# Optimization experiments

Hardware: AMD Instinct MI355X
Metric: run time of the kernel (lower is better)

Reference implementation:

```python
import jax, jax.numpy as jnp
import numpy as np
from jax import lax

B, C, H, W = 4, 512, 64, 64
C8 = C // 8
OUT = 256
BN_EPS = 1e-5


def setup_inputs() -> dict:
    key = jax.random.key(0)
    ks = jax.random.split(key, 12)
    s = lambda k, shape, fan: jax.random.normal(k, shape, jnp.float32) * (1.0 / np.sqrt(fan))
    return {
        "x": jax.random.normal(ks[0], (B, C, H, W), jnp.float32),
        "wq": s(ks[1], (C8, C), C), "bq": jnp.zeros((C8,), jnp.float32),
        "wk": s(ks[2], (C8, C), C), "bk": jnp.zeros((C8,), jnp.float32),
        "wv": s(ks[3], (C, C), C),  "bv": jnp.zeros((C,), jnp.float32),
        "ca_w1": s(ks[4], (C8, C), C),
        "ca_w2": s(ks[5], (C, C8), C8),
        "conv_w": s(ks[6], (OUT, C, 3, 3), C * 9),
        "bn_gamma": jnp.ones((OUT,), jnp.float32),
        "bn_beta": jnp.zeros((OUT,), jnp.float32),
        "bn_mean": jnp.zeros((OUT,), jnp.float32),
        "bn_var": jnp.ones((OUT,), jnp.float32),
    }


def reference(x, wq, bq, wk, bk, wv, bv, ca_w1, ca_w2, conv_w,
              bn_gamma, bn_beta, bn_mean, bn_var):
    b, c, h, w = x.shape
    n = h * w
    xf = x.reshape(b, c, n)  # [B,C,N]

    # ---- Position attention ----
    q = jnp.einsum('qc,bcn->bnq', wq, xf) + bq            # [B,N,C8]
    k = jnp.einsum('kc,bcn->bkn', wk, xf) + bk[:, None]   # [B,C8,N]
    energy = jnp.einsum('bnq,bqm->bnm', q, k)             # [B,N,N]
    attn = jax.nn.softmax(energy, axis=-1)
    v = jnp.einsum('vc,bcn->bvn', wv, xf) + bv[:, None]   # [B,C,N]
    # torch: bmm(value, attention^T) -> out[b,c,m] = sum_n v[b,c,n]*attn[b,m,n]
    pa = jnp.einsum('bcn,bmn->bcm', v, attn).reshape(b, c, h, w) + x

    # ---- Channel attention (SE-style, avg+max pooled, shared MLP) ----
    avg = jnp.mean(pa, axis=(2, 3))   # [B,C]
    mx = jnp.max(pa, axis=(2, 3))     # [B,C]
    fc = lambda z: jnp.einsum('oc,bc->bo', ca_w2,
                              jax.nn.relu(jnp.einsum('hc,bc->bh', ca_w1, z)))
    scale = jax.nn.sigmoid(fc(avg) + fc(mx))[:, :, None, None]
    ca = scale * pa

    # ---- Conv 3x3 + BN (eval mode) + ReLU ----
    y = lax.conv_general_dilated(ca, conv_w, (1, 1), 'SAME',
                                 dimension_numbers=('NCHW', 'OIHW', 'NCHW'))
    inv = lax.rsqrt(bn_var + BN_EPS)
    y = (y - bn_mean[:, None, None]) * (inv * bn_gamma)[:, None, None] + bn_beta[:, None, None]
    return jax.nn.relu(y)
```

## Files before the change

### kernel.cpp

```cpp
#include <hip/hip_runtime.h>

#define NB 4
#define CIN 512
#define NPIX 4096
#define CQK 64
#define COUT 256
#define PPIX 4356

typedef __bf16 bh16;
typedef _Float16 fh16;
typedef __attribute__((ext_vector_type(8))) __bf16 bf16x8;
typedef __attribute__((ext_vector_type(8))) _Float16 f16x8;
typedef __attribute__((ext_vector_type(16))) float f32x16;

#define AS1 __attribute__((address_space(1)))
#define AS3 __attribute__((address_space(3)))

__device__ __forceinline__ void glds16(const void* g, void* l) {
  __builtin_amdgcn_global_load_lds((const AS1 unsigned int*)g, (AS3 unsigned int*)l, 16, 0, 0);
}

__global__ __launch_bounds__(256) void transpose_bf_k(const float* __restrict__ src,
                                                      bh16* __restrict__ dst,
                                                      int rows, int cols) {
  __shared__ float tile[32][33];
  const int b = blockIdx.z;
  const int c0 = blockIdx.x * 32;
  const int r0 = blockIdx.y * 32;
  const float* s = src + (size_t)b * rows * cols;
  bh16* d = dst + (size_t)b * rows * cols;
  const int tx = threadIdx.x, ty = threadIdx.y;
#pragma unroll
  for (int i = 0; i < 32; i += 8)
    tile[ty + i][tx] = s[(size_t)(r0 + ty + i) * cols + (c0 + tx)];
  __syncthreads();
#pragma unroll
  for (int i = 0; i < 32; i += 8)
    d[(size_t)(c0 + ty + i) * rows + (r0 + tx)] = (bh16)tile[tx][ty + i];
}

__global__ __launch_bounds__(256) void wcast_k(const float* __restrict__ wq,
                                               const float* __restrict__ wk,
                                               const float* __restrict__ wv,
                                               const float* __restrict__ bq,
                                               const float* __restrict__ bk,
                                               bh16* __restrict__ Wqk,
                                               bh16* __restrict__ wvb,
                                               float* __restrict__ bias128) {
  const int idx = blockIdx.x * 256 + threadIdx.x;
  if (idx < 65536) {
    Wqk[idx] = (bh16)(idx < 32768 ? wq[idx] : wk[idx - 32768]);
  } else {
    const int j = idx - 65536;
    wvb[j] = (bh16)wv[j];
  }
  if (idx < 128) bias128[idx] = idx < 64 ? bq[idx] : bk[idx - 64];
}

__global__ __launch_bounds__(256) void qk_proj_k(const bh16* __restrict__ xTb,
                                                 const bh16* __restrict__ Wqk,
                                                 const float* __restrict__ bias128,
                                                 bh16* __restrict__ Qb,
                                                 bh16* __restrict__ Kf) {
  const int blk = blockIdx.x;
  const int t = threadIdx.x;
  const int w = t >> 6, l31 = t & 31, hi = (t & 63) >> 5;
  __shared__ __align__(16) bh16 As[2][64 * 64];
  f32x16 acc[2];
#pragma unroll
  for (int nt = 0; nt < 2; nt++)
#pragma unroll
    for (int r = 0; r < 16; r++) acc[nt][r] = 0.0f;

#define QK_STAGE(kc, buf)                                                           \
  {                                                                                 \
    _Pragma("unroll") for (int i = 0; i < 2; i++) {                                 \
      const int s = i * 256 + t;                                                    \
      const int n = s >> 3, slot = s & 7;                                           \
      glds16(xTb + (size_t)(blk * 64 + n) * CIN + (kc) * 64 + (((slot + n) & 7) * 8), \
             &As[buf][(size_t)(i * 256 + w * 64) * 8]);                             \
    }                                                                               \
  }

  QK_STAGE(0, 0);
  __syncthreads();
  for (int kc = 0; kc < 8; kc++) {
    if (kc < 7) QK_STAGE(kc + 1, (kc + 1) & 1);
    const bh16* as = As[kc & 1];
#pragma unroll
    for (int ks = 0; ks < 4; ks++) {
      const bf16x8 bfr = *(const bf16x8*)(Wqk + (size_t)(w * 32 + l31) * CIN + kc * 64 + ks * 16 + hi * 8);
      const int kk = ks * 2 + hi;
#pragma unroll
      for (int nt = 0; nt < 2; nt++) {
        const int n = nt * 32 + l31;
        const bf16x8 a = *(const bf16x8*)&as[(size_t)(n * 8 + ((kk - n) & 7)) * 8];
        acc[nt] = __builtin_amdgcn_mfma_f32_32x32x16_bf16(a, bfr, acc[nt], 0, 0, 0);
      }
    }
    __syncthreads();
  }
#undef QK_STAGE
  const int o = w * 32 + l31;
  const float bo = bias128[o];
  if (w < 2) {
#pragma unroll
    for (int nt = 0; nt < 2; nt++)
#pragma unroll
      for (int r = 0; r < 16; r++) {
        const int nloc = nt * 32 + (r & 3) + 8 * (r >> 2) + 4 * hi;
        Qb[(size_t)(blk * 64 + nloc) * 64 + o] = (bh16)(acc[nt][r] + bo);
      }
  } else {
    const int b = blk >> 6, jtile = blk & 63;
    const int k = o - 64, kg = k >> 3, k7 = k & 7;
    bh16* kdst = Kf + (((size_t)(b * 64 + jtile) * 8 + kg) * 64) * 8 + k7;
#pragma unroll
    for (int nt = 0; nt < 2; nt++)
#pragma unroll
      for (int r = 0; r < 16; r++) {
        const int j = nt * 32 + (r & 3) + 8 * (r >> 2) + 4 * hi;
        kdst[(size_t)j * 8] = (bh16)(acc[nt][r] + bo);
      }
  }
}

__global__ __launch_bounds__(256) void v_proj_k(const bh16* __restrict__ xTb,
                                                const bh16* __restrict__ wvb,
                                                const float* __restrict__ bv,
                                                bh16* __restrict__ Vf) {
  const int nblk = blockIdx.x;
  const int cblk = blockIdx.y;
  const int b = blockIdx.z;
  const int t = threadIdx.x;
  const int w = t >> 6, l31 = t & 31, hi = (t & 63) >> 5;
  __shared__ __align__(16) bh16 Bs[2][256 * 64];
  f32x16 acc[2][2];
#pragma unroll
  for (int mt = 0; mt < 2; mt++)
#pragma unroll
    for (int nt = 0; nt < 2; nt++)
#pragma unroll
      for (int r = 0; r < 16; r++) acc[mt][nt][r] = 0.0f;

#define V_STAGE(kc, buf)                                                              \
  {                                                                                   \
    _Pragma("unroll") for (int i = 0; i < 8; i++) {                                   \
      const int s = i * 256 + t;                                                      \
      const int n = s >> 3, slot = s & 7;                                             \
      glds16(xTb + (size_t)(b * NPIX + nblk * 256 + n) * CIN + (kc) * 64 + (((slot + n) & 7) * 8), \
             &Bs[buf][(size_t)(i * 256 + w * 64) * 8]);                               \
    }                                                                                 \
  }

  V_STAGE(0, 0);
  __syncthreads();
  for (int kc = 0; kc < 8; kc++) {
    if (kc < 7) V_STAGE(kc + 1, (kc + 1) & 1);
    const bh16* bs = Bs[kc & 1];
#pragma unroll
    for (int ks = 0; ks < 4; ks++) {
      const int kk = ks * 2 + hi;
      bf16x8 a[2], bfr[2];
#pragma unroll
      for (int mt = 0; mt < 2; mt++)
        a[mt] = *(const bf16x8*)(wvb + (size_t)(cblk * 64 + mt * 32 + l31) * CIN + kc * 64 + ks * 16 + hi * 8);
#pragma unroll
      for (int nt = 0; nt < 2; nt++) {
        const int n = w * 64 + nt * 32 + l31;
        bfr[nt] = *(const bf16x8*)&bs[(size_t)(n * 8 + ((kk - n) & 7)) * 8];
      }
#pragma unroll
      for (int mt = 0; mt < 2; mt++)
#pragma unroll
        for (int nt = 0; nt < 2; nt++)
          acc[mt][nt] = __builtin_amdgcn_mfma_f32_32x32x16_bf16(a[mt], bfr[nt], acc[mt][nt], 0, 0, 0);
    }
    __syncthreads();
  }
#undef V_STAGE
  const int ntile0 = nblk * 4 + w;
#pragma unroll
  for (int mt = 0; mt < 2; mt++)
#pragma unroll
    for (int r = 0; r < 16; r++) {
      const int c = cblk * 64 + mt * 32 + (r & 3) + 8 * (r >> 2) + 4 * hi;
      const float bvc = bv[c];
#pragma unroll
      for (int nt = 0; nt < 2; nt++) {
        const int nl = nt * 32 + l31;
        Vf[(((size_t)(b * 64 + ntile0) * 8 + (nl >> 3)) * 512 + c) * 8 + (nl & 7)] =
            (bh16)(acc[mt][nt][r] + bvc);
      }
    }
}

__global__ __launch_bounds__(256, 2) void attn1p_k(const bh16* __restrict__ Qb,
                                                   const bh16* __restrict__ Kf,
                                                   const bh16* __restrict__ Vf,
                                                   const float* __restrict__ x,
                                                   float* __restrict__ pa) {
  const int id = blockIdx.x + 2 * (blockIdx.y + 64 * blockIdx.z);
  const int b = (id & 7) >> 1;
  const int cblk = id & 1;
  const int mblk = (id >> 3) * 64;
  const int t = threadIdx.x;
  const int w = t >> 6, l31 = t & 31, hi = (t >> 5) & 1;
  const int jhalf = w & 1, mhalf = w >> 1;
  __shared__ __align__(16) bh16 Ps[2][8 * 64 * 8];
  __shared__ float lred[4][32];
  __shared__ float linvL[64];

  bf16x8 qf[4];
  {
    const bh16* qrow = Qb + (size_t)(b * NPIX + mblk + mhalf * 32 + l31) * 64;
#pragma unroll
    for (int ks = 0; ks < 4; ks++) qf[ks] = *(const bf16x8*)(qrow + ks * 16 + hi * 8);
  }
  const bh16* kfb = Kf + (size_t)b * (64 * 8 * 64 * 8);
  const bh16* vfb = Vf + (size_t)b * (64 * 8 * 512 * 8);
  const int cbase = cblk * 256 + w * 64;

  f32x16 acc[2][2];
#pragma unroll
  for (int mt = 0; mt < 2; mt++)
#pragma unroll
    for (int ct = 0; ct < 2; ct++)
#pragma unroll
      for (int r = 0; r < 16; r++) acc[mt][ct][r] = 0.0f;
  float lsum = 0.0f;

  bf16x8 kf[4], vf[4][2];
#pragma unroll
  for (int ks = 0; ks < 4; ks++) {
    kf[ks] = *(const bf16x8*)(kfb + (((size_t)0 * 8 + ks * 2 + hi) * 64 + jhalf * 32 + l31) * 8);
#pragma unroll
    for (int ct = 0; ct < 2; ct++)
      vf[ks][ct] = *(const bf16x8*)(vfb + (((size_t)0 * 8 + ks * 2 + hi) * 512 + cbase + ct * 32 + l31) * 8);
  }

  for (int it = 0; it < 64; it++) {
    f32x16 s1;
#pragma unroll
    for (int r = 0; r < 16; r++) s1[r] = 0.0f;
#pragma unroll
    for (int ks = 0; ks < 4; ks++)
      s1 = __builtin_amdgcn_mfma_f32_32x32x16_bf16(kf[ks], qf[ks], s1, 0, 0, 0);
    bf16x8 kfn[4], vfn[4][2];
    if (it < 63) {
      const size_t nt1 = (size_t)(it + 1) * 8;
#pragma unroll
      for (int ks = 0; ks < 4; ks++) {
        kfn[ks] = *(const bf16x8*)(kfb + ((nt1 + ks * 2 + hi) * 64 + jhalf * 32 + l31) * 8);
#pragma unroll
        for (int ct = 0; ct < 2; ct++)
          vfn[ks][ct] = *(const bf16x8*)(vfb + ((nt1 + ks * 2 + hi) * 512 + cbase + ct * 32 + l31) * 8);
      }
    }
    bh16* psw = Ps[it & 1];
#pragma unroll
    for (int g = 0; g < 4; g++) {
      union { bh16 h[4]; uint2 u2; } pk;
#pragma unroll
      for (int q = 0; q < 4; q++) {
        const float p = __expf(s1[g * 4 + q]);
        lsum += p;
        pk.h[q] = (bh16)p;
      }
      *(uint2*)(void*)&psw[(size_t)((jhalf * 4 + g) * 64 + mhalf * 32 + l31) * 8 + hi * 4] = pk.u2;
    }
    __syncthreads();
    const bh16* ps = Ps[it & 1];
#pragma unroll
    for (int ks = 0; ks < 4; ks++) {
      bf16x8 pf[2];
#pragma unroll
      for (int mt = 0; mt < 2; mt++)
        pf[mt] = *(const bf16x8*)&ps[(size_t)((ks * 2 + hi) * 64 + mt * 32 + l31) * 8];
#pragma unroll
      for (int mt = 0; mt < 2; mt++)
#pragma unroll
        for (int ct = 0; ct < 2; ct++)
          acc[mt][ct] = __builtin_amdgcn_mfma_f32_32x32x16_bf16(pf[mt], vf[ks][ct], acc[mt][ct], 0, 0, 0);
    }
#pragma unroll
    for (int ks = 0; ks < 4; ks++) {
      kf[ks] = kfn[ks];
      vf[ks][0] = vfn[ks][0];
      vf[ks][1] = vfn[ks][1];
    }
  }

  lsum += __shfl_xor(lsum, 32);
  if (hi == 0) lred[w][l31] = lsum;
  __syncthreads();
  if (t < 64) linvL[t] = 1.0f / (lred[(t >> 5) * 2][t & 31] + lred[(t >> 5) * 2 + 1][t & 31]);
  __syncthreads();

#pragma unroll
  for (int mt = 0; mt < 2; mt++) {
#pragma unroll
    for (int g = 0; g < 4; g++) {
      const int mloc = mt * 32 + g * 8 + hi * 4;
      const float4 lv = *(const float4*)&linvL[mloc];
#pragma unroll
      for (int ct = 0; ct < 2; ct++) {
        const size_t base = (size_t)(b * CIN + cblk * 256 + w * 64 + ct * 32 + l31) * NPIX + mblk + mloc;
        const float4 xv = *(const float4*)&x[base];
        float4 r;
        r.x = acc[mt][ct][g * 4 + 0] * lv.x + xv.x;
        r.y = acc[mt][ct][g * 4 + 1] * lv.y + xv.y;
        r.z = acc[mt][ct][g * 4 + 2] * lv.z + xv.z;
        r.w = acc[mt][ct][g * 4 + 3] * lv.w + xv.w;
        *(float4*)&pa[base] = r;
      }
    }
  }
}

__global__ __launch_bounds__(256) void pool2_k(const float* __restrict__ pa,
                                               float* __restrict__ avgv,
                                               float* __restrict__ maxv) {
  const int t = threadIdx.x;
  const int row = blockIdx.x * 4 + (t >> 6);
  const int lane = t & 63;
  const float* base = pa + (size_t)row * NPIX;
  float s = 0.0f, mx = -1e30f;
#pragma unroll
  for (int i = 0; i < 16; i++) {
    const float4 v = *(const float4*)(base + i * 256 + lane * 4);
    s += v.x + v.y + v.z + v.w;
    mx = fmaxf(mx, fmaxf(fmaxf(v.x, v.y), fmaxf(v.z, v.w)));
  }
#pragma unroll
  for (int d = 1; d < 64; d <<= 1) {
    s += __shfl_xor(s, d);
    mx = fmaxf(mx, __shfl_xor(mx, d));
  }
  if (lane == 0) {
    avgv[row] = s * (1.0f / 4096.0f);
    maxv[row] = mx;
  }
}

__global__ __launch_bounds__(256) void mlp2_k(const float* __restrict__ avgv,
                                              const float* __restrict__ maxv,
                                              const float* __restrict__ w1,
                                              const float* __restrict__ w2,
                                              float* __restrict__ scale) {
  const int b = blockIdx.x;
  const int t = threadIdx.x;
  __shared__ float avg_l[CIN], max_l[CIN], hbuf[128];
#pragma unroll
  for (int h = 0; h < 2; h++) {
    const int c = t + h * 256;
    avg_l[c] = avgv[b * CIN + c];
    max_l[c] = maxv[b * CIN + c];
  }
  __syncthreads();
  if (t < 128) {
    const float* src = (t < 64) ? avg_l : max_l;
    const int o = t & 63;
    float sacc = 0.0f;
    for (int c = 0; c < CIN; c++) sacc += w1[o * CIN + c] * src[c];
    hbuf[t] = fmaxf(sacc, 0.0f);
  }
  __syncthreads();
#pragma unroll
  for (int h = 0; h < 2; h++) {
    const int c = t + h * 256;
    float sacc = 0.0f;
#pragma unroll
    for (int k = 0; k < 64; k++) sacc += w2[c * 64 + k] * (hbuf[k] + hbuf[64 + k]);
    scale[b * CIN + c] = 1.0f / (1.0f + __expf(-sacc));
  }
}

__global__ __launch_bounds__(256) void pack_k(const float* __restrict__ pa,
                                              const float* __restrict__ scl,
                                              fh16* __restrict__ pab) {
  __shared__ float tile[32][65];
  const int n0 = blockIdx.x * 32;
  const int c0 = blockIdx.y * 64;
  const int b = blockIdx.z;
  const int t = threadIdx.x;
  {
    const int px = t & 31, cc = t >> 5;
#pragma unroll
    for (int i = 0; i < 8; i++) {
      const int c = cc * 8 + i;
      tile[px][c] = pa[((size_t)(b * CIN + c0 + c)) * NPIX + n0 + px] * scl[b * CIN + c0 + c];
    }
  }
  __syncthreads();
  {
    const int pixr = t >> 5, c2 = (t & 31) * 2;
#pragma unroll
    for (int j = 0; j < 4; j++) {
      const int pix = pixr + j * 8;
      const int n = n0 + pix;
      const int pp = ((n >> 6) + 1) * 66 + (n & 63) + 1;
      union { fh16 h[2]; unsigned int u; } pk;
      pk.h[0] = (fh16)tile[pix][c2];
      pk.h[1] = (fh16)tile[pix][c2 + 1];
      *(unsigned int*)(void*)(pab + ((size_t)b * PPIX + pp) * CIN + c0 + c2) = pk.u;
    }
  }
}

__global__ __launch_bounds__(256) void wpack_k(const float* __restrict__ cw,
                                               fh16* __restrict__ wp) {
  const int d0 = (blockIdx.x * 256 + threadIdx.x) * 8;
  const int cc = d0 & 15;
  const int q = d0 >> 4;
  const int o = q & 63;
  const int q2 = q >> 6;
  const int tap = q2 % 9;
  const int q3 = q2 / 9;
  const int chunk = q3 & 31;
  const int oblk = q3 >> 5;
  const size_t sbase = (size_t)(oblk * 64 + o) * 4608 + (size_t)(chunk * 16 + cc) * 9 + tap;
  union { fh16 h[8]; uint4 u4; } pk;
#pragma unroll
  for (int i = 0; i < 8; i++) pk.h[i] = (fh16)cw[sbase + (size_t)i * 9];
  *(uint4*)(void*)(wp + d0) = pk.u4;
}

__global__ __launch_bounds__(256) void conv_mfma_k(const fh16* __restrict__ pab,
                                                   const fh16* __restrict__ wp,
                                                   const float* __restrict__ gamma,
                                                   const float* __restrict__ beta,
                                                   const float* __restrict__ mean,
                                                   const float* __restrict__ var,
                                                   float* __restrict__ out) {
  const int y0 = blockIdx.x * 4;
  const int oblk = blockIdx.y;
  const int b = blockIdx.z;
  const int t = threadIdx.x;
  const int w = t >> 6, lane = t & 63, l31 = lane & 31, hi = lane >> 5;
  __shared__ __align__(16) fh16 Xs[2][416 * 16];
  __shared__ __align__(16) fh16 Ws[2][9 * 64 * 16];
  __shared__ float sb[64], bb[64];
  if (t < 64) {
    const int o = oblk * 64 + t;
    const float inv = rsqrtf(var[o] + 1e-5f);
    const float sc = inv * gamma[o];
    sb[t] = sc;
    bb[t] = beta[o] - mean[o] * sc;
  }
  f32x16 o00, o01, o10, o11;
#pragma unroll
  for (int r = 0; r < 16; r++) { o00[r] = 0.0f; o01[r] = 0.0f; o10[r] = 0.0f; o11[r] = 0.0f; }

  const fh16* xbase = pab + ((size_t)b * PPIX + y0 * 66) * CIN + (lane >> 1) * CIN + (lane & 1) * 8;
  const fh16* wbase = wp + (size_t)oblk * 32 * 9216 + lane * 8;

#define STAGE(chunk, buf)                                                        \
  {                                                                              \
    const fh16* xs = xbase + (chunk) * 16;                                       \
    for (int i = w; i < 13; i += 4)                                              \
      glds16(xs + (size_t)i * 32 * CIN, &Xs[buf][i * 512]);                      \
    const fh16* wsrc = wbase + (size_t)(chunk) * 9216;                           \
    for (int i = w; i < 18; i += 4)                                              \
      glds16(wsrc + (size_t)i * 512, &Ws[buf][i * 512]);                         \
  }

  STAGE(0, 0);
  __syncthreads();
  for (int chunk = 0; chunk < 32; chunk++) {
    if (chunk < 31) STAGE(chunk + 1, (chunk + 1) & 1);
    const fh16* xs = Xs[chunk & 1];
    const fh16* ws = Ws[chunk & 1];
#pragma unroll
    for (int tap = 0; tap < 9; tap++) {
      const int ky = tap / 3, kx = tap - ky * 3;
      const f16x8 a0 = *(const f16x8*)&ws[tap * 1024 + l31 * 16 + hi * 8];
      const f16x8 a1 = *(const f16x8*)&ws[tap * 1024 + (32 + l31) * 16 + hi * 8];
      const int px = ((w + ky) * 66 + l31 + kx) * 16 + hi * 8;
      const f16x8 b0 = *(const f16x8*)&xs[px];
      const f16x8 b1 = *(const f16x8*)&xs[px + 32 * 16];
      o00 = __builtin_amdgcn_mfma_f32_32x32x16_f16(a0, b0, o00, 0, 0, 0);
      o01 = __builtin_amdgcn_mfma_f32_32x32x16_f16(a0, b1, o01, 0, 0, 0);
      o10 = __builtin_amdgcn_mfma_f32_32x32x16_f16(a1, b0, o10, 0, 0, 0);
      o11 = __builtin_amdgcn_mfma_f32_32x32x16_f16(a1, b1, o11, 0, 0, 0);
    }
    __syncthreads();
  }
#undef STAGE

  const f32x16* accs[2][2] = {{&o00, &o01}, {&o10, &o11}};
#pragma unroll
  for (int mt = 0; mt < 2; mt++) {
#pragma unroll
    for (int nt = 0; nt < 2; nt++) {
      const f32x16& A = *accs[mt][nt];
#pragma unroll
      for (int r = 0; r < 16; r++) {
        const int cl = mt * 32 + (r & 3) + 8 * (r >> 2) + 4 * hi;
        const int pix = nt * 32 + l31;
        const float y = A[r] * sb[cl] + bb[cl];
        out[((size_t)(b * COUT + oblk * 64 + cl)) * NPIX + (y0 + w) * 64 + pix] = fmaxf(y, 0.0f);
      }
    }
  }
}

extern "C" void kernel_launch(void* const* d_in, const int* in_sizes, int n_in,
                              void* d_out, int out_size, void* d_ws, size_t ws_size,
                              hipStream_t stream) {
  (void)in_sizes; (void)n_in; (void)out_size; (void)ws_size;
  const float* x        = (const float*)d_in[0];
  const float* wq       = (const float*)d_in[1];
  const float* bq       = (const float*)d_in[2];
  const float* wk       = (const float*)d_in[3];
  const float* bk       = (const float*)d_in[4];
  const float* wv       = (const float*)d_in[5];
  const float* bv       = (const float*)d_in[6];
  const float* ca_w1    = (const float*)d_in[7];
  const float* ca_w2    = (const float*)d_in[8];
  const float* conv_w   = (const float*)d_in[9];
  const float* bn_gamma = (const float*)d_in[10];
  const float* bn_beta  = (const float*)d_in[11];
  const float* bn_mean  = (const float*)d_in[12];
  const float* bn_var   = (const float*)d_in[13];
  float* out = (float*)d_out;

  float* ws = (float*)d_ws;
  float* pa      = ws;
  bh16*  Vf      = (bh16*)(ws + 8388608);
  fh16*  wpck    = (fh16*)(ws + 8388608);
  bh16*  Qb      = (bh16*)(ws + 12582912);
  bh16*  Kf      = (bh16*)(ws + 13107200);
  bh16*  xTb     = (bh16*)(ws + 13631488);
  fh16*  pab     = (fh16*)(ws + 13631488);
  bh16*  Wqk     = (bh16*)(ws + 17825792);
  bh16*  wvb     = (bh16*)(ws + 17858560);
  float* bias128 = ws + 17989632;
  float* avgv    = ws + 18100224;
  float* maxv    = ws + 18102272;
  float* scl     = ws + 18104320;

  wcast_k<<<dim3(1280, 1, 1), 256, 0, stream>>>(wq, wk, wv, bq, bk, Wqk, wvb, bias128);
  transpose_bf_k<<<dim3(NPIX / 32, CIN / 32, NB), dim3(32, 8, 1), 0, stream>>>(x, xTb, CIN, NPIX);
  qk_proj_k<<<dim3(256, 1, 1), 256, 0, stream>>>(xTb, Wqk, bias128, Qb, Kf);
  v_proj_k<<<dim3(16, 8, NB), 256, 0, stream>>>(xTb, wvb, bv, Vf);
  attn1p_k<<<dim3(2, 64, NB), 256, 0, stream>>>(Qb, Kf, Vf, x, pa);
  hipMemsetAsync(pab, 0, (size_t)(NB * PPIX * CIN + 16384) * sizeof(fh16), stream);
  pool2_k<<<dim3(512, 1, 1), 256, 0, stream>>>(pa, avgv, maxv);
  mlp2_k<<<dim3(NB, 1, 1), 256, 0, stream>>>(avgv, maxv, ca_w1, ca_w2, scl);
  pack_k<<<dim3(NPIX / 32, CIN / 64, NB), 256, 0, stream>>>(pa, scl, pab);
  wpack_k<<<dim3(576, 1, 1), 256, 0, stream>>>(conv_w, wpck);
  conv_mfma_k<<<dim3(16, 4, NB), 256, 0, stream>>>(pab, wpck, bn_gamma, bn_beta,
                                                   bn_mean, bn_var, out);
}
```

Measured before the change: 341.8 us.

## Software-pipeline attention loop: overlap exp/P-write with PV MFMAs, deepen K prefetch

Restructures the position-attention main loop into a skewed software pipeline. The QK score MFMA for the next tile runs ahead, and the exp/softmax packing of the current tile is interleaved with the PV MFMAs of the previous tile. K fragments are prefetched two tiles ahead and V one tile ahead. The aim is to hide exp latency and global load latency behind matrix-core work, leaving one barrier per iteration. The cost is more live registers (extra s1, K and V buffers), which may lower occupancy or cause spills, plus an epilogue to drain the last PV tile.

```diff
diff --git a/kernel.cpp b/kernel.cpp
--- a/kernel.cpp
+++ b/kernel.cpp
@@ -221,6 +221,9 @@
   const bh16* vfb = Vf + (size_t)b * (64 * 8 * 512 * 8);
   const int cbase = cblk * 256 + w * 64;
 
+#define KADDR(tile, ks) (kfb + (((size_t)(tile) * 8 + (ks) * 2 + hi) * 64 + jhalf * 32 + l31) * 8)
+#define VADDR(tile, ks, ct) (vfb + (((size_t)(tile) * 8 + (ks) * 2 + hi) * 512 + cbase + (ct) * 32 + l31) * 8)
+
   f32x16 acc[2][2];
 #pragma unroll
   for (int mt = 0; mt < 2; mt++)
@@ -230,66 +233,100 @@
       for (int r = 0; r < 16; r++) acc[mt][ct][r] = 0.0f;
   float lsum = 0.0f;
 
-  bf16x8 kf[4], vf[4][2];
-#pragma unroll
-  for (int ks = 0; ks < 4; ks++) {
-    kf[ks] = *(const bf16x8*)(kfb + (((size_t)0 * 8 + ks * 2 + hi) * 64 + jhalf * 32 + l31) * 8);
-#pragma unroll
-    for (int ct = 0; ct < 2; ct++)
-      vf[ks][ct] = *(const bf16x8*)(vfb + (((size_t)0 * 8 + ks * 2 + hi) * 512 + cbase + ct * 32 + l31) * 8);
+  bf16x8 kf_nxt[4], kf_fly[4];
+  bf16x8 vf_use[4][2], vf_rdy[4][2];
+  f32x16 s1;
+  {
+    bf16x8 k0[4];
+#pragma unroll
+    for (int ks = 0; ks < 4; ks++) {
+      k0[ks] = *(const bf16x8*)KADDR(0, ks);
+#pragma unroll
+      for (int ct = 0; ct < 2; ct++) vf_rdy[ks][ct] = *(const bf16x8*)VADDR(0, ks, ct);
+    }
+#pragma unroll
+    for (int ks = 0; ks < 4; ks++) {
+      kf_nxt[ks] = *(const bf16x8*)KADDR(1, ks);
+      kf_fly[ks] = *(const bf16x8*)KADDR(2, ks);
+    }
+#pragma unroll
+    for (int r = 0; r < 16; r++) s1[r] = 0.0f;
+#pragma unroll
+    for (int ks = 0; ks < 4; ks++)
+      s1 = __builtin_amdgcn_mfma_f32_32x32x16_bf16(k0[ks], qf[ks], s1, 0, 0, 0);
   }
 
   for (int it = 0; it < 64; it++) {
-    f32x16 s1;
-#pragma unroll
-    for (int r = 0; r < 16; r++) s1[r] = 0.0f;
+    f32x16 s1n;
+#pragma unroll
+    for (int r = 0; r < 16; r++) s1n[r] = 0.0f;
 #pragma unroll
     for (int ks = 0; ks < 4; ks++)
-      s1 = __builtin_amdgcn_mfma_f32_32x32x16_bf16(kf[ks], qf[ks], s1, 0, 0, 0);
-    bf16x8 kfn[4], vfn[4][2];
-    if (it < 63) {
-      const size_t nt1 = (size_t)(it + 1) * 8;
+      s1n = __builtin_amdgcn_mfma_f32_32x32x16_bf16(kf_nxt[ks], qf[ks], s1n, 0, 0, 0);
+
+    const bh16* ps = Ps[(it + 1) & 1];
+    bh16* psw = Ps[it & 1];
+    if (it) {
 #pragma unroll
       for (int ks = 0; ks < 4; ks++) {
-        kfn[ks] = *(const bf16x8*)(kfb + ((nt1 + ks * 2 + hi) * 64 + jhalf * 32 + l31) * 8);
-#pragma unroll
-        for (int ct = 0; ct < 2; ct++)
-          vfn[ks][ct] = *(const bf16x8*)(vfb + ((nt1 + ks * 2 + hi) * 512 + cbase + ct * 32 + l31) * 8);
-      }
-    }
-    bh16* psw = Ps[it & 1];
-#pragma unroll
-    for (int g = 0; g < 4; g++) {
-      union { bh16 h[4]; uint2 u2; } pk;
-#pragma unroll
-      for (int q = 0; q < 4; q++) {
-        const float p = __expf(s1[g * 4 + q]);
-        lsum += p;
-        pk.h[q] = (bh16)p;
-      }
-      *(uint2*)(void*)&psw[(size_t)((jhalf * 4 + g) * 64 + mhalf * 32 + l31) * 8 + hi * 4] = pk.u2;
+        bf16x8 pf0 = *(const bf16x8*)&ps[(size_t)((ks * 2 + hi) * 64 + l31) * 8];
+        bf16x8 pf1 = *(const bf16x8*)&ps[(size_t)((ks * 2 + hi) * 64 + 32 + l31) * 8];
+        acc[0][0] = __builtin_amdgcn_mfma_f32_32x32x16_bf16(pf0, vf_use[ks][0], acc[0][0], 0, 0, 0);
+        acc[0][1] = __builtin_amdgcn_mfma_f32_32x32x16_bf16(pf0, vf_use[ks][1], acc[0][1], 0, 0, 0);
+        {
+          union { bh16 h[4]; uint2 u2; } pk;
+#pragma unroll
+          for (int q = 0; q < 4; q++) {
+            const float p = __expf(s1[ks * 4 + q]);
+            lsum += p;
+            pk.h[q] = (bh16)p;
+          }
+          *(uint2*)(void*)&psw[(size_t)((jhalf * 4 + ks) * 64 + mhalf * 32 + l31) * 8 + hi * 4] = pk.u2;
+        }
+        acc[1][0] = __builtin_amdgcn_mfma_f32_32x32x16_bf16(pf1, vf_use[ks][0], acc[1][0], 0, 0, 0);
+        acc[1][1] = __builtin_amdgcn_mfma_f32_32x32x16_bf16(pf1, vf_use[ks][1], acc[1][1], 0, 0, 0);
+      }
+    } else {
+#pragma unroll
+      for (int g = 0; g < 4; g++) {
+        union { bh16 h[4]; uint2 u2; } pk;
+#pragma unroll
+        for (int q = 0; q < 4; q++) {
+          const float p = __expf(s1[g * 4 + q]);
+          lsum += p;
+          pk.h[q] = (bh16)p;
+        }
+        *(uint2*)(void*)&psw[(size_t)((jhalf * 4 + g) * 64 + mhalf * 32 + l31) * 8 + hi * 4] = pk.u2;
+      }
     }
     __syncthreads();
-    const bh16* ps = Ps[it & 1];
+    s1 = s1n;
+    const int kt = (it + 3 < 64) ? it + 3 : 63;
+    const int vt = (it + 1 < 64) ? it + 1 : 63;
 #pragma unroll
     for (int ks = 0; ks < 4; ks++) {
-      bf16x8 pf[2];
-#pragma unroll
-      for (int mt = 0; mt < 2; mt++)
-        pf[mt] = *(const bf16x8*)&ps[(size_t)((ks * 2 + hi) * 64 + mt * 32 + l31) * 8];
-#pragma unroll
-      for (int mt = 0; mt < 2; mt++)
-#pragma unroll
-        for (int ct = 0; ct < 2; ct++)
-          acc[mt][ct] = __builtin_amdgcn_mfma_f32_32x32x16_bf16(pf[mt], vf[ks][ct], acc[mt][ct], 0, 0, 0);
-    }
+      kf_nxt[ks] = kf_fly[ks];
+      kf_fly[ks] = *(const bf16x8*)KADDR(kt, ks);
+      vf_use[ks][0] = vf_rdy[ks][0];
+      vf_use[ks][1] = vf_rdy[ks][1];
+      vf_rdy[ks][0] = *(const bf16x8*)VADDR(vt, ks, 0);
+      vf_rdy[ks][1] = *(const bf16x8*)VADDR(vt, ks, 1);
+    }
+  }
+  {
+    const bh16* ps = Ps[1];
 #pragma unroll
     for (int ks = 0; ks < 4; ks++) {
-      kf[ks] = kfn[ks];
-      vf[ks][0] = vfn[ks][0];
-      vf[ks][1] = vfn[ks][1];
-    }
-  }
+      bf16x8 pf0 = *(const bf16x8*)&ps[(size_t)((ks * 2 + hi) * 64 + l31) * 8];
+      bf16x8 pf1 = *(const bf16x8*)&ps[(size_t)((ks * 2 + hi) * 64 + 32 + l31) * 8];
+      acc[0][0] = __builtin_amdgcn_mfma_f32_32x32x16_bf16(pf0, vf_use[ks][0], acc[0][0], 0, 0, 0);
+      acc[0][1] = __builtin_amdgcn_mfma_f32_32x32x16_bf16(pf0, vf_use[ks][1], acc[0][1], 0, 0, 0);
+      acc[1][0] = __builtin_amdgcn_mfma_f32_32x32x16_bf16(pf1, vf_use[ks][0], acc[1][0], 0, 0, 0);
+      acc[1][1] = __builtin_amdgcn_mfma_f32_32x32x16_bf16(pf1, vf_use[ks][1], acc[1][1], 0, 0, 0);
+    }
+  }
+#undef KADDR
+#undef VADDR
 
   lsum += __shfl_xor(lsum, 32);
   if (hi == 0) lred[w][l31] = lsum;
```

Measured after the change: 339.7 us. No clear change (-0.6%).
